# Optimization experiments

Measured on AMD Instinct MI355X. Metric: run time of the kernel, lower is better.

The kernel has to match this reference:

```python
import jax, jax.numpy as jnp
import numpy as np
from itertools import product

# problem dims
B, D = 2, 80            # batch, grid side -> 2*80^3 = 1.024M voxel slots
N = 200000
CIN, COUT = 32, 64
KV = 27                 # 3x3x3 kernel volume


def _build_rulebook():
    """Submanifold conv rulebook: in_idx[k, j] = input row whose coord equals
    coord_j + offset_k, or N (zero pad row) if that voxel is empty/out of grid."""
    rng = np.random.default_rng(0)
    total = B * D ** 3
    flat = rng.choice(total, size=N, replace=False)
    b, rem = flat // D ** 3, flat % D ** 3
    x, y, z = rem // (D * D), (rem // D) % D, rem % D
    lookup = np.full(total, N, dtype=np.int64)  # empty -> pad index N
    lookup[flat] = np.arange(N)
    rows = []
    for dx, dy, dz in product((-1, 0, 1), repeat=3):  # kernel offsets, dilation=1
        nx, ny, nz = x + dx, y + dy, z + dz
        valid = (0 <= nx) & (nx < D) & (0 <= ny) & (ny < D) & (0 <= nz) & (nz < D)
        nflat = ((b * D + nx) * D + ny) * D + nz
        rows.append(np.where(valid, lookup[np.clip(nflat, 0, total - 1)], N))
    return np.stack(rows).astype(np.int32)  # [KV, N]


def setup_inputs() -> dict:
    key = jax.random.key(0)
    k1, k2, k3 = jax.random.split(key, 3)
    stdv = 1.0 / float(np.sqrt(CIN * KV))  # matches reset_parameters
    feats = jax.random.normal(k1, (N, CIN), dtype=jnp.float32)
    weight = jax.random.uniform(k2, (KV, CIN, COUT), jnp.float32, -stdv, stdv)
    bias = jax.random.uniform(k3, (COUT,), jnp.float32, -stdv, stdv)
    in_idx = jnp.asarray(_build_rulebook())
    return {"feats": feats, "weight": weight, "bias": bias, "in_idx": in_idx}


def reference(feats, weight, bias, in_idx):
    # pad row N = zeros so missing neighbors contribute nothing
    feats_pad = jnp.concatenate(
        [feats, jnp.zeros((1, feats.shape[1]), feats.dtype)], axis=0)  # [N+1, Cin]

    def body(acc, kw):  # scan over the 27 kernel offsets: gather -> matmul -> accumulate
        idx_k, w_k = kw                       # [N] int32, [Cin, Cout]
        return acc + feats_pad[idx_k] @ w_k, None

    out0 = jnp.zeros((feats.shape[0], weight.shape[2]), feats.dtype)  # [N, Cout]
    out, _ = jax.lax.scan(body, out0, (in_idx, weight))
    return out + bias
```

## Files before the change

### kernel.cpp

```cpp
#include <hip/hip_runtime.h>
#include <cstddef>
#include <cstdint>

#define NROWS 200000
#define CIN   32
#define COUT  64
#define KV    27

typedef __attribute__((ext_vector_type(8))) short  short8;
typedef __attribute__((ext_vector_type(4))) float  f32x4;

__device__ __forceinline__ unsigned short f2bf(float x) {
  unsigned u = __builtin_bit_cast(unsigned, x);
  u += 0x7FFFu + ((u >> 16) & 1u);
  return (unsigned short)(u >> 16);
}

__global__ void prep_weight_kernel(const float* __restrict__ w,
                                   short8* __restrict__ wsB) {
  int tid = blockIdx.x * blockDim.x + threadIdx.x;
  if (tid >= KV * 4 * 64) return;
  int lane = tid & 63;
  int t    = (tid >> 6) & 3;
  int k    = tid >> 8;
  int col  = t * 16 + (lane & 15);
  int kin0 = (lane >> 4) * 8;
  short8 v;
#pragma unroll
  for (int f = 0; f < 8; ++f)
    v[f] = (short)f2bf(w[((size_t)k * CIN + kin0 + f) * COUT + col]);
  wsB[tid] = v;
}

__global__ void prep_feats_kernel(const float* __restrict__ feats,
                                  short8* __restrict__ fb) {
  int i = blockIdx.x * blockDim.x + threadIdx.x;
  const int total8 = (NROWS + 1) * CIN / 8;
  if (i >= total8) return;
  short8 v = {0, 0, 0, 0, 0, 0, 0, 0};
  if (i < NROWS * CIN / 8) {
    const f32x4* p = (const f32x4*)feats + (size_t)i * 2;
    f32x4 a = p[0], b = p[1];
#pragma unroll
    for (int f = 0; f < 4; ++f) {
      v[f]     = (short)f2bf(a[f]);
      v[4 + f] = (short)f2bf(b[f]);
    }
  }
  fb[i] = v;
}

template <int MODE>
__global__ __launch_bounds__(256)
void spconv_mfma_kernel(const float* __restrict__ feats,
                        const unsigned short* __restrict__ featsbf,
                        const short8* __restrict__ wsB,
                        const float* __restrict__ bias,
                        const int* __restrict__ in_idx,
                        float* __restrict__ out) {
  const int lane = threadIdx.x & 63;
  const int wid  = (int)((blockIdx.x * blockDim.x + threadIdx.x) >> 6);
  if (wid >= NROWS / 64) return;
  const int row0 = wid * 64;
  const int c16  = lane & 15;
  const int kg   = lane >> 4;

  f32x4 acc[4][4];
#pragma unroll
  for (int t = 0; t < 4; ++t) {
    float bv = bias[t * 16 + c16];
    f32x4 bvv = {bv, bv, bv, bv};
#pragma unroll
    for (int m = 0; m < 4; ++m) acc[m][t] = bvv;
  }

  for (int k = 0; k < KV; ++k) {
    short8 bfr[4];
#pragma unroll
    for (int t = 0; t < 4; ++t) bfr[t] = wsB[(k * 4 + t) * 64 + lane];
#pragma unroll
    for (int m = 0; m < 4; ++m) {
      const int idx = in_idx[(size_t)k * NROWS + row0 + m * 16 + c16];
      short8 afr;
      if (MODE == 0) {
        afr = *(const short8*)(featsbf + (size_t)idx * CIN + kg * 8);
      } else {
        short8 z = {0, 0, 0, 0, 0, 0, 0, 0};
        afr = z;
        if (idx < NROWS) {
          const f32x4* p = (const f32x4*)(feats + (size_t)idx * CIN + kg * 8);
          f32x4 a = p[0], b = p[1];
#pragma unroll
          for (int f = 0; f < 4; ++f) {
            afr[f]     = (short)f2bf(a[f]);
            afr[4 + f] = (short)f2bf(b[f]);
          }
        }
      }
#pragma unroll
      for (int t = 0; t < 4; ++t)
        acc[m][t] = __builtin_amdgcn_mfma_f32_16x16x32_bf16(afr, bfr[t], acc[m][t], 0, 0, 0);
    }
  }

#pragma unroll
  for (int m = 0; m < 4; ++m)
#pragma unroll
    for (int t = 0; t < 4; ++t)
#pragma unroll
      for (int r = 0; r < 4; ++r)
        out[(size_t)(row0 + m * 16 + kg * 4 + r) * COUT + t * 16 + c16] = acc[m][t][r];
}

__global__ void spconv_naive_kernel(const float* __restrict__ feats,
                                    const float* __restrict__ w,
                                    const float* __restrict__ bias,
                                    const int* __restrict__ in_idx,
                                    float* __restrict__ out) {
  int gid = blockIdx.x * blockDim.x + threadIdx.x;
  if (gid >= NROWS * COUT) return;
  int row = gid / COUT, co = gid % COUT;
  float acc = bias[co];
  for (int k = 0; k < KV; ++k) {
    int idx = in_idx[(size_t)k * NROWS + row];
    if (idx < NROWS) {
      const float* fr = feats + (size_t)idx * CIN;
      const float* wk = w + (size_t)k * CIN * COUT + co;
#pragma unroll
      for (int c = 0; c < CIN; ++c) acc += fr[c] * wk[(size_t)c * COUT];
    }
  }
  out[gid] = acc;
}

extern "C" void kernel_launch(void* const* d_in, const int* in_sizes, int n_in,
                              void* d_out, int out_size, void* d_ws, size_t ws_size,
                              hipStream_t stream) {
  const float* feats  = (const float*)d_in[0];
  const float* weight = (const float*)d_in[1];
  const float* bias   = (const float*)d_in[2];
  const int*   in_idx = (const int*)d_in[3];
  float*       out    = (float*)d_out;

  const size_t wsB_bytes = (size_t)KV * 4 * 64 * 16;
  const size_t fb_bytes  = (size_t)(NROWS + 1) * CIN * 2;
  short8*         wsB     = (short8*)d_ws;
  unsigned short* featsbf = (unsigned short*)((char*)d_ws + wsB_bytes);

  const int nwave      = NROWS / 64;
  const int mainBlocks = (nwave * 64 + 255) / 256;

  if (ws_size >= wsB_bytes + fb_bytes) {
    prep_weight_kernel<<<27, 256, 0, stream>>>(weight, wsB);
    prep_feats_kernel<<<((NROWS + 1) * CIN / 8 + 255) / 256, 256, 0, stream>>>(
        feats, (short8*)featsbf);
    spconv_mfma_kernel<0><<<mainBlocks, 256, 0, stream>>>(
        feats, featsbf, wsB, bias, in_idx, out);
  } else if (ws_size >= wsB_bytes) {
    prep_weight_kernel<<<27, 256, 0, stream>>>(weight, wsB);
    spconv_mfma_kernel<1><<<mainBlocks, 256, 0, stream>>>(
        feats, featsbf, wsB, bias, in_idx, out);
  } else {
    spconv_naive_kernel<<<(NROWS * COUT + 255) / 256, 256, 0, stream>>>(
        feats, weight, bias, in_idx, out);
  }
}
```

Before: 59.16 us.

## Stage weights in LDS, shrink per-wave tile to 16 rows, prefetch gathers

The main kernel now gives each wave 16 output rows instead of 64 and launches 1024-thread blocks, so there are four times as many waves to hide gather latency. Each block copies the full bf16 weight fragment table into shared memory once. The loop software-pipelines the indexed feature gathers, loading indices two offsets ahead and feature rows one offset ahead. The costs are a large per-block LDS footprint (about 110 KB) that limits blocks per CU, a weight copy repeated in every block, and a weight fragment loaded per MFMA with no reuse across row tiles. The fallback path for a workspace that only fits the weights is removed.

```diff
diff --git a/kernel.cpp b/kernel.cpp
--- a/kernel.cpp
+++ b/kernel.cpp
@@ -50,66 +50,64 @@
   fb[i] = v;
 }
 
-template <int MODE>
-__global__ __launch_bounds__(256)
-void spconv_mfma_kernel(const float* __restrict__ feats,
-                        const unsigned short* __restrict__ featsbf,
+__global__ __launch_bounds__(1024, 4)
+void spconv_mfma_kernel(const unsigned short* __restrict__ featsbf,
                         const short8* __restrict__ wsB,
                         const float* __restrict__ bias,
                         const int* __restrict__ in_idx,
                         float* __restrict__ out) {
-  const int lane = threadIdx.x & 63;
-  const int wid  = (int)((blockIdx.x * blockDim.x + threadIdx.x) >> 6);
-  if (wid >= NROWS / 64) return;
-  const int row0 = wid * 64;
-  const int c16  = lane & 15;
-  const int kg   = lane >> 4;
+  __shared__ short8 sB[KV * 4 * 64];
 
-  f32x4 acc[4][4];
+  const int tid = threadIdx.x;
+  for (int i = tid; i < KV * 4 * 64; i += 1024) sB[i] = wsB[i];
+  __syncthreads();
+
+  const int lane = tid & 63;
+  const int wid  = (int)((blockIdx.x * 1024 + tid) >> 6);
+  const int row0 = wid * 16;
+  if (row0 >= NROWS) return;
+  const int c16 = lane & 15;
+  const int kg  = lane >> 4;
+
+  f32x4 acc[4];
 #pragma unroll
   for (int t = 0; t < 4; ++t) {
     float bv = bias[t * 16 + c16];
     f32x4 bvv = {bv, bv, bv, bv};
-#pragma unroll
-    for (int m = 0; m < 4; ++m) acc[m][t] = bvv;
+    acc[t] = bvv;
   }
 
+  const int* idxp = in_idx + row0 + c16;
+  const unsigned short* fb = featsbf;
+  const int koff = kg * 8;
+
+  int idA = idxp[0];
+  int idB = idxp[(size_t)1 * NROWS];
+  short8 af = *(const short8*)(fb + (size_t)idA * CIN + koff);
+
   for (int k = 0; k < KV; ++k) {
-    short8 bfr[4];
-#pragma unroll
-    for (int t = 0; t < 4; ++t) bfr[t] = wsB[(k * 4 + t) * 64 + lane];
-#pragma unroll
-    for (int m = 0; m < 4; ++m) {
-      const int idx = in_idx[(size_t)k * NROWS + row0 + m * 16 + c16];
-      short8 afr;
-      if (MODE == 0) {
-        afr = *(const short8*)(featsbf + (size_t)idx * CIN + kg * 8);
-      } else {
-        short8 z = {0, 0, 0, 0, 0, 0, 0, 0};
-        afr = z;
-        if (idx < NROWS) {
-          const f32x4* p = (const f32x4*)(feats + (size_t)idx * CIN + kg * 8);
-          f32x4 a = p[0], b = p[1];
-#pragma unroll
-          for (int f = 0; f < 4; ++f) {
-            afr[f]     = (short)f2bf(a[f]);
-            afr[4 + f] = (short)f2bf(b[f]);
-          }
-        }
-      }
-#pragma unroll
-      for (int t = 0; t < 4; ++t)
-        acc[m][t] = __builtin_amdgcn_mfma_f32_16x16x32_bf16(afr, bfr[t], acc[m][t], 0, 0, 0);
-    }
+    const int kk2 = (k + 2 < KV) ? k + 2 : KV - 1;
+    int idC = idxp[(size_t)kk2 * NROWS];
+    short8 afn = *(const short8*)(fb + (size_t)idB * CIN + koff);
+
+    short8 b0 = sB[(k * 4 + 0) * 64 + lane];
+    short8 b1 = sB[(k * 4 + 1) * 64 + lane];
+    short8 b2 = sB[(k * 4 + 2) * 64 + lane];
+    short8 b3 = sB[(k * 4 + 3) * 64 + lane];
+
+    acc[0] = __builtin_amdgcn_mfma_f32_16x16x32_bf16(af, b0, acc[0], 0, 0, 0);
+    acc[1] = __builtin_amdgcn_mfma_f32_16x16x32_bf16(af, b1, acc[1], 0, 0, 0);
+    acc[2] = __builtin_amdgcn_mfma_f32_16x16x32_bf16(af, b2, acc[2], 0, 0, 0);
+    acc[3] = __builtin_amdgcn_mfma_f32_16x16x32_bf16(af, b3, acc[3], 0, 0, 0);
+
+    af = afn; idA = idB; idB = idC;
   }
 
 #pragma unroll
-  for (int m = 0; m < 4; ++m)
+  for (int t = 0; t < 4; ++t)
 #pragma unroll
-    for (int t = 0; t < 4; ++t)
-#pragma unroll
-      for (int r = 0; r < 4; ++r)
-        out[(size_t)(row0 + m * 16 + kg * 4 + r) * COUT + t * 16 + c16] = acc[m][t][r];
+    for (int r = 0; r < 4; ++r)
+      out[(size_t)(row0 + kg * 4 + r) * COUT + t * 16 + c16] = acc[t][r];
 }
 
 __global__ void spconv_naive_kernel(const float* __restrict__ feats,
@@ -147,19 +145,13 @@
   short8*         wsB     = (short8*)d_ws;
   unsigned short* featsbf = (unsigned short*)((char*)d_ws + wsB_bytes);
 
-  const int nwave      = NROWS / 64;
-  const int mainBlocks = (nwave * 64 + 255) / 256;
-
   if (ws_size >= wsB_bytes + fb_bytes) {
     prep_weight_kernel<<<27, 256, 0, stream>>>(weight, wsB);
     prep_feats_kernel<<<((NROWS + 1) * CIN / 8 + 255) / 256, 256, 0, stream>>>(
         feats, (short8*)featsbf);
-    spconv_mfma_kernel<0><<<mainBlocks, 256, 0, stream>>>(
-        feats, featsbf, wsB, bias, in_idx, out);
-  } else if (ws_size >= wsB_bytes) {
-    prep_weight_kernel<<<27, 256, 0, stream>>>(weight, wsB);
-    spconv_mfma_kernel<1><<<mainBlocks, 256, 0, stream>>>(
-        feats, featsbf, wsB, bias, in_idx, out);
+    const int blocks = (NROWS + 255) / 256;
+    spconv_mfma_kernel<<<blocks, 1024, 0, stream>>>(
+        featsbf, wsB, bias, in_idx, out);
   } else {
     spconv_naive_kernel<<<(NROWS * COUT + 255) / 256, 256, 0, stream>>>(
         feats, weight, bias, in_idx, out);
```

New measurement: 74.71 us. 26.3% more time.

## Software-pipeline index and feature gathers across kernel offsets with one-wave blocks

Applied to the files above, without the earlier changes.

Restructures the main MFMA loop as a multi-stage software pipeline. Rulebook indices are prefetched four offsets ahead, gathered bf16 feature fragments two offsets ahead, and weight fragments one offset ahead, so gather latency overlaps the MFMAs. Launches one 64-thread wave per block with launch bounds (64,3) and drops the fp32-gather fallback path. The cost is higher register pressure from the extra in-flight buffers, which may limit occupancy.

```diff
diff --git a/kernel.cpp b/kernel.cpp
--- a/kernel.cpp
+++ b/kernel.cpp
@@ -50,20 +50,17 @@
   fb[i] = v;
 }
 
-template <int MODE>
-__global__ __launch_bounds__(256)
-void spconv_mfma_kernel(const float* __restrict__ feats,
-                        const unsigned short* __restrict__ featsbf,
+__global__ __launch_bounds__(64, 3)
+void spconv_mfma_kernel(const unsigned short* __restrict__ featsbf,
                         const short8* __restrict__ wsB,
                         const float* __restrict__ bias,
                         const int* __restrict__ in_idx,
                         float* __restrict__ out) {
   const int lane = threadIdx.x & 63;
-  const int wid  = (int)((blockIdx.x * blockDim.x + threadIdx.x) >> 6);
-  if (wid >= NROWS / 64) return;
-  const int row0 = wid * 64;
+  const int row0 = blockIdx.x << 6;
   const int c16  = lane & 15;
   const int kg   = lane >> 4;
+  const int koff = kg * 8;
 
   f32x4 acc[4][4];
 #pragma unroll
@@ -74,33 +71,58 @@
     for (int m = 0; m < 4; ++m) acc[m][t] = bvv;
   }
 
+  const int*   idxp = in_idx + row0 + c16;
+  const short8* bp  = wsB + lane;
+
+  int i0[4], i1[4], ic[4], id_[4];
+#pragma unroll
+  for (int m = 0; m < 4; ++m) i0[m]  = idxp[(size_t)0 * NROWS + m * 16];
+#pragma unroll
+  for (int m = 0; m < 4; ++m) i1[m]  = idxp[(size_t)1 * NROWS + m * 16];
+#pragma unroll
+  for (int m = 0; m < 4; ++m) ic[m]  = idxp[(size_t)2 * NROWS + m * 16];
+#pragma unroll
+  for (int m = 0; m < 4; ++m) id_[m] = idxp[(size_t)3 * NROWS + m * 16];
+
+  short8 af0[4], af1[4];
+#pragma unroll
+  for (int m = 0; m < 4; ++m)
+    af0[m] = *(const short8*)(featsbf + (size_t)i0[m] * CIN + koff);
+#pragma unroll
+  for (int m = 0; m < 4; ++m)
+    af1[m] = *(const short8*)(featsbf + (size_t)i1[m] * CIN + koff);
+
+  short8 bc0 = bp[0], bc1 = bp[64], bc2 = bp[128], bc3 = bp[192];
+
   for (int k = 0; k < KV; ++k) {
-    short8 bfr[4];
+    const int kb = (k + 1 < KV) ? k + 1 : KV - 1;
+    short8 bn0 = bp[(kb * 4 + 0) * 64], bn1 = bp[(kb * 4 + 1) * 64],
+           bn2 = bp[(kb * 4 + 2) * 64], bn3 = bp[(kb * 4 + 3) * 64];
+
+    const int ki = (k + 4 < KV) ? k + 4 : KV - 1;
+    int it[4];
 #pragma unroll
-    for (int t = 0; t < 4; ++t) bfr[t] = wsB[(k * 4 + t) * 64 + lane];
+    for (int m = 0; m < 4; ++m) it[m] = idxp[(size_t)ki * NROWS + m * 16];
+
+    short8 ag[4];
+#pragma unroll
+    for (int m = 0; m < 4; ++m)
+      ag[m] = *(const short8*)(featsbf + (size_t)ic[m] * CIN + koff);
+
 #pragma unroll
     for (int m = 0; m < 4; ++m) {
-      const int idx = in_idx[(size_t)k * NROWS + row0 + m * 16 + c16];
-      short8 afr;
-      if (MODE == 0) {
-        afr = *(const short8*)(featsbf + (size_t)idx * CIN + kg * 8);
-      } else {
-        short8 z = {0, 0, 0, 0, 0, 0, 0, 0};
-        afr = z;
-        if (idx < NROWS) {
-          const f32x4* p = (const f32x4*)(feats + (size_t)idx * CIN + kg * 8);
-          f32x4 a = p[0], b = p[1];
+      acc[m][0] = __builtin_amdgcn_mfma_f32_16x16x32_bf16(af0[m], bc0, acc[m][0], 0, 0, 0);
+      acc[m][1] = __builtin_amdgcn_mfma_f32_16x16x32_bf16(af0[m], bc1, acc[m][1], 0, 0, 0);
+      acc[m][2] = __builtin_amdgcn_mfma_f32_16x16x32_bf16(af0[m], bc2, acc[m][2], 0, 0, 0);
+      acc[m][3] = __builtin_amdgcn_mfma_f32_16x16x32_bf16(af0[m], bc3, acc[m][3], 0, 0, 0);
+    }
+
 #pragma unroll
-          for (int f = 0; f < 4; ++f) {
-            afr[f]     = (short)f2bf(a[f]);
-            afr[4 + f] = (short)f2bf(b[f]);
-          }
-        }
-      }
-#pragma unroll
-      for (int t = 0; t < 4; ++t)
-        acc[m][t] = __builtin_amdgcn_mfma_f32_16x16x32_bf16(afr, bfr[t], acc[m][t], 0, 0, 0);
+    for (int m = 0; m < 4; ++m) {
+      af0[m] = af1[m]; af1[m] = ag[m];
+      ic[m] = id_[m]; id_[m] = it[m];
     }
+    bc0 = bn0; bc1 = bn1; bc2 = bn2; bc3 = bn3;
   }
 
 #pragma unroll
@@ -147,19 +169,13 @@
   short8*         wsB     = (short8*)d_ws;
   unsigned short* featsbf = (unsigned short*)((char*)d_ws + wsB_bytes);
 
-  const int nwave      = NROWS / 64;
-  const int mainBlocks = (nwave * 64 + 255) / 256;
-
   if (ws_size >= wsB_bytes + fb_bytes) {
     prep_weight_kernel<<<27, 256, 0, stream>>>(weight, wsB);
     prep_feats_kernel<<<((NROWS + 1) * CIN / 8 + 255) / 256, 256, 0, stream>>>(
         feats, (short8*)featsbf);
-    spconv_mfma_kernel<0><<<mainBlocks, 256, 0, stream>>>(
-        feats, featsbf, wsB, bias, in_idx, out);
-  } else if (ws_size >= wsB_bytes) {
-    prep_weight_kernel<<<27, 256, 0, stream>>>(weight, wsB);
-    spconv_mfma_kernel<1><<<mainBlocks, 256, 0, stream>>>(
-        feats, featsbf, wsB, bias, in_idx, out);
+    const int blocks = NROWS / 64;
+    spconv_mfma_kernel<<<blocks, 64, 0, stream>>>(
+        featsbf, wsB, bias, in_idx, out);
   } else {
     spconv_naive_kernel<<<(NROWS * COUT + 255) / 256, 256, 0, stream>>>(
         feats, weight, bias, in_idx, out);
```

Measured after the change: 71.66 us. 1.21x slower.
